# Kernel tuning notes

Hardware: AMD Instinct MI355X
Metric: run time of the kernel (lower is better)

The kernel has to match this reference:

```python
import jax, jax.numpy as jnp
import numpy as np

N = 32768   # total nodes
B = 128     # graphs
L = 256     # nodes per graph (equal-size graphs -> pad_sequence == reshape)
F = 768     # num_features
NH = 256    # nhid
H = 128     # lstm hidden per direction (nhid // 2)
E = 524288  # edges
C = 2       # num_classes


def setup_inputs() -> dict:
    key = jax.random.key(0)
    ks = jax.random.split(key, 16)
    def w(k, shape, fan_in):
        return jax.random.normal(k, shape, jnp.float32) / np.sqrt(fan_in)
    x = jax.random.normal(ks[0], (N, F), jnp.float32)
    edge_index = jax.random.randint(ks[1], (2, E), 0, N)
    batch = jnp.repeat(jnp.arange(B), L)  # sorted graph ids, L nodes per graph
    return {
        "x": x,
        "edge_index": edge_index,
        "batch": batch,
        "W_gcn": w(ks[2], (F, NH), F),
        "b_gcn": jnp.zeros((NH,), jnp.float32),
        # LSTM layer 0: [dir, 4H, Din], gate order i,f,g,o (PyTorch)
        "lstm0_Wih": w(ks[3], (2, 4 * H, F), F),
        "lstm0_Whh": w(ks[4], (2, 4 * H, H), H),
        "lstm0_b": jnp.zeros((2, 4 * H), jnp.float32),
        # LSTM layer 1: input = 2H (bidirectional concat)
        "lstm1_Wih": w(ks[5], (2, 4 * H, 2 * H), 2 * H),
        "lstm1_Whh": w(ks[6], (2, 4 * H, H), H),
        "lstm1_b": jnp.zeros((2, 4 * H), jnp.float32),
        "W_seq": w(ks[7], (NH, NH), NH),
        "b_seq": jnp.zeros((NH,), jnp.float32),
        "W1": w(ks[8], (2 * NH, NH), 2 * NH),
        "b1": jnp.zeros((NH,), jnp.float32),
        "W2": w(ks[9], (NH, C), NH),
        "b2": jnp.zeros((C,), jnp.float32),
    }


def _lstm_dir(xs, Wih, Whh, b, reverse):
    # xs: [Bt, L, Din] -> hidden seq [Bt, L, H]
    Hh = Whh.shape[-1]
    def step(carry, xt):
        h, c = carry
        g = xt @ Wih.T + h @ Whh.T + b
        i, f, gg, o = jnp.split(g, 4, axis=-1)
        c = jax.nn.sigmoid(f) * c + jax.nn.sigmoid(i) * jnp.tanh(gg)
        h = jax.nn.sigmoid(o) * jnp.tanh(c)
        return (h, c), h
    x_t = jnp.swapaxes(xs, 0, 1)  # [L, Bt, Din]
    init = (jnp.zeros((xs.shape[0], Hh), xs.dtype),
            jnp.zeros((xs.shape[0], Hh), xs.dtype))
    _, hs = jax.lax.scan(step, init, x_t, reverse=reverse)
    return jnp.swapaxes(hs, 0, 1)


def _lstm_bidir(xs, Wih, Whh, b):
    fwd = _lstm_dir(xs, Wih[0], Whh[0], b[0], False)
    bwd = _lstm_dir(xs, Wih[1], Whh[1], b[1], True)
    return jnp.concatenate([fwd, bwd], axis=-1)


def reference(x, edge_index, batch, W_gcn, b_gcn,
              lstm0_Wih, lstm0_Whh, lstm0_b,
              lstm1_Wih, lstm1_Whh, lstm1_b,
              W_seq, b_seq, W1, b1, W2, b2):
    n = x.shape[0]
    # --- GCNConv (add self loops, symmetric norm) ---
    loops = jnp.arange(n)
    row = jnp.concatenate([edge_index[0], loops])
    col = jnp.concatenate([edge_index[1], loops])
    deg = jax.ops.segment_sum(jnp.ones_like(col, x.dtype), col, num_segments=n)
    dinv = jnp.where(deg > 0, jax.lax.rsqrt(deg), 0.0)
    norm = dinv[row] * dinv[col]
    h = x @ W_gcn                                   # [N, NH]
    agg = jax.ops.segment_sum(h[row] * norm[:, None], col, num_segments=n)
    x_graph = jax.nn.relu(agg + b_gcn)
    # --- global max pool per graph ---
    x_graph = jax.ops.segment_max(x_graph, batch, num_segments=B)  # [B, NH]
    # --- unbatch + pad_sequence (equal-size graphs -> reshape) ---
    seq_x = x.reshape(B, L, F)
    # --- bidirectional 2-layer LSTM ---
    seq_x = _lstm_bidir(seq_x, lstm0_Wih, lstm0_Whh, lstm0_b)  # [B, L, 2H]
    seq_x = _lstm_bidir(seq_x, lstm1_Wih, lstm1_Whh, lstm1_b)  # [B, L, 2H]
    seq_x = seq_x[:, 0, :]                                      # pre_padding=False -> first step
    # dropout is identity in eval mode
    x_seq = jax.nn.leaky_relu(seq_x @ W_seq + b_seq, negative_slope=0.01)
    out = jnp.concatenate([x_graph, x_seq], axis=1)             # [B, 2*NH]
    out = jax.nn.relu(out @ W1 + b1)
    return jax.nn.log_softmax(out @ W2 + b2, axis=-1)
```

## Files before the change

### kernel.cpp

```cpp
#include <hip/hip_runtime.h>
#include <math.h>


namespace {

constexpr int kN  = 32768;
constexpr int kB  = 128;
constexpr int kL  = 256;
constexpr int kF  = 768;
constexpr int kNH = 256;
constexpr int kH  = 128;
constexpr int kE  = 524288;

typedef __attribute__((ext_vector_type(8))) short bf16x8;
typedef __attribute__((ext_vector_type(4))) float f32x4;
typedef __attribute__((address_space(3))) unsigned int lds_u32;
typedef __attribute__((address_space(1))) unsigned int glb_u32;

__device__ __forceinline__ float sigf(float x)  { return 1.f / (1.f + __expf(-x)); }
__device__ __forceinline__ float tanh_f(float x){ return 1.f - 2.f / (1.f + __expf(2.f * x)); }

__device__ __forceinline__ unsigned short f2bf(float f) {
  unsigned int u = __float_as_uint(f);
  u = u + 0x7fffu + ((u >> 16) & 1u);
  return (unsigned short)(u >> 16);
}
__device__ __forceinline__ float bf2f(unsigned short h) {
  return __uint_as_float((unsigned int)h << 16);
}


__global__ void count_edges(const int* __restrict__ col, int* __restrict__ cnt) {
  int e = blockIdx.x * 256 + threadIdx.x;
  if (e < kE) atomicAdd(&cnt[col[e]], 1);
}

__global__ void scan_dinv(const int* __restrict__ cnt, int* __restrict__ offs,
                          int* __restrict__ cursor, float* __restrict__ dinv) {
  __shared__ int part[1024];
  int t = threadIdx.x;
  int base = t * 32;
  int loc[32];
  int s = 0;
#pragma unroll
  for (int i = 0; i < 32; i++) { loc[i] = cnt[base + i]; s += loc[i]; }
  part[t] = s;
  __syncthreads();
  for (int d = 1; d < 1024; d <<= 1) {
    int v = part[t];
    int add = (t >= d) ? part[t - d] : 0;
    __syncthreads();
    part[t] = v + add;
    __syncthreads();
  }
  int run = (t == 0) ? 0 : part[t - 1];
#pragma unroll
  for (int i = 0; i < 32; i++) {
    offs[base + i] = run;
    cursor[base + i] = run;
    dinv[base + i] = rsqrtf((float)(loc[i] + 1));
    run += loc[i];
  }
  if (t == 1023) offs[kN] = run;
}

__global__ void fill_csr(const int* __restrict__ row, const int* __restrict__ col,
                         int* __restrict__ cursor, int* __restrict__ elist) {
  int e = blockIdx.x * 256 + threadIdx.x;
  if (e < kE) {
    int c = col[e];
    int p = atomicAdd(&cursor[c], 1);
    elist[p] = row[e];
  }
}


__global__ void convert_bt(const float* __restrict__ W, unsigned short* __restrict__ hi,
                           unsigned short* __restrict__ lo, int Nn, int Kk, int trans) {
  int idx = blockIdx.x * 256 + threadIdx.x;
  if (idx >= Nn * Kk) return;
  int n = idx / Kk, k = idx - n * Kk;
  float f = trans ? W[(size_t)k * Nn + n] : W[idx];
  unsigned short h = f2bf(f);
  hi[idx] = h;
  lo[idx] = f2bf(f - bf2f(h));
}

__global__ __launch_bounds__(256, 2) void gemm3(const float* __restrict__ A,
                                                const unsigned short* __restrict__ Bhi,
                                                const unsigned short* __restrict__ Blo,
                                                float* __restrict__ C,
                                                int M, int N, int K) {
  __shared__ __align__(16) char lds[32768];
  const int tid = threadIdx.x;
  const int lane = tid & 63;
  const int w = tid >> 6, wr = w >> 1, wc = w & 1;
  const int m0 = blockIdx.y * 128, n0 = blockIdx.x * 128;

  f32x4 acc[4][4];
#pragma unroll
  for (int i = 0; i < 4; i++)
#pragma unroll
    for (int j = 0; j < 4; j++) acc[i][j] = (f32x4)0.f;

  const float* aptr[4];
  int aoff[4];
#pragma unroll
  for (int i = 0; i < 4; i++) {
    int f = tid + i * 256;
    int row = f >> 3, kq4 = f & 7;
    aptr[i] = A + (size_t)(m0 + row) * K + kq4 * 4;
    int sub = row >> 4, r = row & 15, q = kq4 >> 1, hs = kq4 & 1;
    aoff[i] = sub * 1024 + (q * 16 + r) * 16 + hs * 8;
  }
  const unsigned short* bsrc[4];
  int boff[4];
#pragma unroll
  for (int j = 0; j < 4; j++) {
    int id = w * 4 + j;
    int isLo = id >> 3, sub = id & 7;
    const unsigned short* Bp = isLo ? Blo : Bhi;
    bsrc[j] = Bp + (size_t)(n0 + sub * 16 + (lane & 15)) * K + (lane >> 4) * 8;
    boff[j] = 16384 + isLo * 8192 + sub * 1024;
  }

  for (int k0 = 0; k0 < K; k0 += 32) {
#pragma unroll
    for (int j = 0; j < 4; j++) {
      __builtin_amdgcn_global_load_lds((const glb_u32*)bsrc[j],
                                       (lds_u32*)(lds + boff[j]), 16, 0, 0);
      bsrc[j] += 32;
    }
#pragma unroll
    for (int i = 0; i < 4; i++) {
      f32x4 v = *(const f32x4*)(aptr[i]);
      aptr[i] += 32;
      unsigned short h0 = f2bf(v.x), h1 = f2bf(v.y), h2 = f2bf(v.z), h3 = f2bf(v.w);
      unsigned short g0 = f2bf(v.x - bf2f(h0)), g1 = f2bf(v.y - bf2f(h1));
      unsigned short g2 = f2bf(v.z - bf2f(h2)), g3 = f2bf(v.w - bf2f(h3));
      uint2 hv, lv;
      hv.x = (unsigned int)h0 | ((unsigned int)h1 << 16);
      hv.y = (unsigned int)h2 | ((unsigned int)h3 << 16);
      lv.x = (unsigned int)g0 | ((unsigned int)g1 << 16);
      lv.y = (unsigned int)g2 | ((unsigned int)g3 << 16);
      *(uint2*)(lds + aoff[i]) = hv;
      *(uint2*)(lds + aoff[i] + 8192) = lv;
    }
    __syncthreads();

    const bf16x8* L = (const bf16x8*)lds;
    bf16x8 ah[4], al[4], bh[4], bl[4];
#pragma unroll
    for (int m = 0; m < 4; m++) {
      ah[m] = L[(wr * 4 + m) * 64 + lane];
      al[m] = L[512 + (wr * 4 + m) * 64 + lane];
    }
#pragma unroll
    for (int n = 0; n < 4; n++) {
      bh[n] = L[1024 + (wc * 4 + n) * 64 + lane];
      bl[n] = L[1536 + (wc * 4 + n) * 64 + lane];
    }
#pragma unroll
    for (int m = 0; m < 4; m++)
#pragma unroll
      for (int n = 0; n < 4; n++) {
        acc[m][n] = __builtin_amdgcn_mfma_f32_16x16x32_bf16(ah[m], bh[n], acc[m][n], 0, 0, 0);
        acc[m][n] = __builtin_amdgcn_mfma_f32_16x16x32_bf16(ah[m], bl[n], acc[m][n], 0, 0, 0);
        acc[m][n] = __builtin_amdgcn_mfma_f32_16x16x32_bf16(al[m], bh[n], acc[m][n], 0, 0, 0);
      }
    __syncthreads();
  }

#pragma unroll
  for (int m = 0; m < 4; m++)
#pragma unroll
    for (int n = 0; n < 4; n++) {
      int r0 = m0 + wr * 64 + m * 16 + (lane >> 4) * 4;
      int cc = n0 + wc * 64 + n * 16 + (lane & 15);
#pragma unroll
      for (int j = 0; j < 4; j++)
        C[(size_t)(r0 + j) * N + cc] = acc[m][n][j];
    }
}


__global__ __launch_bounds__(256) void gcn_gather(const float* __restrict__ hg,
                                                  const int* __restrict__ offs,
                                                  const int* __restrict__ elist,
                                                  const float* __restrict__ dinv,
                                                  const float* __restrict__ bgcn,
                                                  float* __restrict__ out) {
  int n = blockIdx.x, j = threadIdx.x;
  float di = dinv[n];
  float acc = hg[(size_t)n * kNH + j] * (di * di);
  int s = offs[n], e = offs[n + 1];
  int p = s;
  for (; p + 4 <= e; p += 4) {
    int r0 = elist[p], r1 = elist[p + 1], r2 = elist[p + 2], r3 = elist[p + 3];
    float w0 = di * dinv[r0], w1 = di * dinv[r1], w2 = di * dinv[r2], w3 = di * dinv[r3];
    float v0 = hg[(size_t)r0 * kNH + j], v1 = hg[(size_t)r1 * kNH + j];
    float v2 = hg[(size_t)r2 * kNH + j], v3 = hg[(size_t)r3 * kNH + j];
    acc = fmaf(v0, w0, acc); acc = fmaf(v1, w1, acc);
    acc = fmaf(v2, w2, acc); acc = fmaf(v3, w3, acc);
  }
  for (; p < e; p++) {
    int r = elist[p];
    acc = fmaf(hg[(size_t)r * kNH + j], di * dinv[r], acc);
  }
  acc += bgcn[j];
  out[(size_t)n * kNH + j] = fmaxf(acc, 0.f);
}

__global__ __launch_bounds__(256) void segmax(const float* __restrict__ xg_full,
                                              float* __restrict__ x_graph) {
  int g = blockIdx.x, j = threadIdx.x;
  const float* base = xg_full + (size_t)g * kL * kNH + j;
  float m0 = -1e30f, m1 = -1e30f, m2 = -1e30f, m3 = -1e30f;
  for (int t = 0; t < kL; t += 4) {
    m0 = fmaxf(m0, base[(size_t)(t + 0) * kNH]);
    m1 = fmaxf(m1, base[(size_t)(t + 1) * kNH]);
    m2 = fmaxf(m2, base[(size_t)(t + 2) * kNH]);
    m3 = fmaxf(m3, base[(size_t)(t + 3) * kNH]);
  }
  x_graph[g * kNH + j] = fmaxf(fmaxf(m0, m1), fmaxf(m2, m3));
}


__global__ __launch_bounds__(512, 2) void lstm_rec(const float* __restrict__ Z, int zstride,
                                                   const float* __restrict__ Whh2,
                                                   const float* __restrict__ bias2,
                                                   float* __restrict__ Y0,
                                                   float* __restrict__ hfin, int mode) {
  __shared__ __align__(16) float hbuf[kH];
  __shared__ float gbuf[512];
  int b, dir;
  if (mode == 0) { dir = blockIdx.x >> 7; b = blockIdx.x & 127; }
  else           { dir = 1;               b = blockIdx.x; }
  const bool rev = (dir == 1);
  int g = threadIdx.x;

  const float* wrow = Whh2 + (size_t)dir * 512 * kH + (size_t)g * kH;
  float w[kH];
#pragma unroll
  for (int k = 0; k < kH / 4; k++) {
    float4 v = *(const float4*)(wrow + 4 * k);
    w[4 * k + 0] = v.x; w[4 * k + 1] = v.y; w[4 * k + 2] = v.z; w[4 * k + 3] = v.w;
  }
  float bg = bias2[dir * 512 + g];
  int zcol = (mode == 0) ? dir * 512 : 0;

  if (g < kH) hbuf[g] = 0.f;
  float c = 0.f;
  __syncthreads();

  const float* zp = Z + (size_t)(b * kL + (rev ? kL - 1 : 0)) * zstride + zcol + g;
  long zinc = rev ? -(long)zstride : (long)zstride;
  float zt = *zp;

  for (int t = 0; t < kL; t++) {
    int tt = rev ? (kL - 1 - t) : t;
    float znext = 0.f;
    if (t < kL - 1) znext = zp[zinc];
    zp += zinc;

    float acc = zt + bg;
#pragma unroll
    for (int kk = 0; kk < kH / 4; kk++) {
      float4 h4 = *(const float4*)&hbuf[kk * 4];
      acc = fmaf(w[4 * kk + 0], h4.x, acc);
      acc = fmaf(w[4 * kk + 1], h4.y, acc);
      acc = fmaf(w[4 * kk + 2], h4.z, acc);
      acc = fmaf(w[4 * kk + 3], h4.w, acc);
    }
    float a = (g < 256 || g >= 384) ? sigf(acc) : tanh_f(acc);
    gbuf[g] = a;
    __syncthreads();
    if (g < kH) {
      float ig = gbuf[g], fg = gbuf[kH + g], gg = gbuf[2 * kH + g], og = gbuf[3 * kH + g];
      c = fg * c + ig * gg;
      float hn = og * tanh_f(c);
      hbuf[g] = hn;
      if (mode == 0) Y0[(size_t)(b * kL + tt) * kNH + dir * kH + g] = hn;
    }
    __syncthreads();
    zt = znext;
  }
  if (mode == 1 && g < kH) hfin[b * kH + g] = hbuf[g];
}


__global__ __launch_bounds__(256) void head(const float* __restrict__ Y0,
                                            const float* __restrict__ h1b,
                                            const float* __restrict__ Wih1f,
                                            const float* __restrict__ b1f,
                                            const float* __restrict__ xgraph,
                                            const float* __restrict__ Wseq,
                                            const float* __restrict__ bseq,
                                            const float* __restrict__ W1,
                                            const float* __restrict__ b1,
                                            const float* __restrict__ W2,
                                            const float* __restrict__ b2,
                                            float* __restrict__ out) {
  int b = blockIdx.x, t = threadIdx.x;
  __shared__ __align__(16) float x0[kNH];
  __shared__ float gl[512];
  __shared__ __align__(16) float seq[kNH];
  __shared__ __align__(16) float v[512];
  __shared__ __align__(16) float o1[kNH];
  __shared__ float red[512];

  x0[t] = Y0[(size_t)(b * kL) * kNH + t];
  if (t >= kH) seq[t] = h1b[b * kH + (t - kH)];
  __syncthreads();

#pragma unroll
  for (int half = 0; half < 2; half++) {
    int g = t + half * 256;
    const float* wr = Wih1f + (size_t)g * kNH;
    float acc = b1f[g];
#pragma unroll 8
    for (int k = 0; k < kNH; k += 4) {
      float4 xv = *(const float4*)&x0[k];
      float4 wv = *(const float4*)(wr + k);
      acc = fmaf(xv.x, wv.x, acc); acc = fmaf(xv.y, wv.y, acc);
      acc = fmaf(xv.z, wv.z, acc); acc = fmaf(xv.w, wv.w, acc);
    }
    gl[g] = acc;
  }
  __syncthreads();
  if (t < kH) {
    float ig = sigf(gl[t]);
    float gg = tanh_f(gl[2 * kH + t]);
    float og = sigf(gl[3 * kH + t]);
    float c = ig * gg;
    seq[t] = og * tanh_f(c);
  }
  v[t] = xgraph[b * kNH + t];
  __syncthreads();

  {
    float acc = bseq[t];
#pragma unroll 4
    for (int k = 0; k < kNH; k++) acc = fmaf(seq[k], Wseq[(size_t)k * kNH + t], acc);
    v[kNH + t] = (acc > 0.f) ? acc : 0.01f * acc;
  }
  __syncthreads();

  {
    float acc = b1[t];
#pragma unroll 4
    for (int k = 0; k < 512; k++) acc = fmaf(v[k], W1[(size_t)k * kNH + t], acc);
    o1[t] = fmaxf(acc, 0.f);
  }
  __syncthreads();

  red[t]       = o1[t] * W2[t * 2 + 0];
  red[kNH + t] = o1[t] * W2[t * 2 + 1];
  __syncthreads();
  for (int s = 128; s > 0; s >>= 1) {
    if (t < s) { red[t] += red[t + s]; red[kNH + t] += red[kNH + t + s]; }
    __syncthreads();
  }
  if (t == 0) {
    float z0 = red[0] + b2[0], z1 = red[kNH] + b2[1];
    float m = fmaxf(z0, z1);
    float lse = m + logf(__expf(z0 - m) + __expf(z1 - m));
    out[b * 2 + 0] = z0 - lse;
    out[b * 2 + 1] = z1 - lse;
  }
}

}

extern "C" void kernel_launch(void* const* d_in, const int* in_sizes, int n_in,
                              void* d_out, int out_size, void* d_ws, size_t ws_size,
                              hipStream_t stream) {
  const float* x     = (const float*)d_in[0];
  const int*   ei    = (const int*)d_in[1];
  const float* Wgcn  = (const float*)d_in[3];
  const float* bgcn  = (const float*)d_in[4];
  const float* l0Wih = (const float*)d_in[5];
  const float* l0Whh = (const float*)d_in[6];
  const float* l0b   = (const float*)d_in[7];
  const float* l1Wih = (const float*)d_in[8];
  const float* l1Whh = (const float*)d_in[9];
  const float* l1b   = (const float*)d_in[10];
  const float* Wseq  = (const float*)d_in[11];
  const float* bseq  = (const float*)d_in[12];
  const float* W1    = (const float*)d_in[13];
  const float* b1    = (const float*)d_in[14];
  const float* W2    = (const float*)d_in[15];
  const float* b2    = (const float*)d_in[16];
  float* out = (float*)d_out;
  char* ws = (char*)d_ws;

  float* Z0     = (float*)(ws);
  float* Y0     = (float*)(ws + 134217728UL);
  float* xgraph = (float*)(ws + 134217728UL + 33554432UL);
  float* h1b    = (float*)(ws + 134217728UL + 33554432UL + 131072UL);
  float* hgcn   = Z0;
  float* xgfull = (float*)(ws + 33554432UL);
  int*   cnt    = (int*)(ws + 67108864UL);
  int*   offs   = (int*)(ws + 67108864UL + 1048576UL);
  int*   cursor = (int*)(ws + 67108864UL + 2097152UL);
  int*   elist  = (int*)(ws + 67108864UL + 3145728UL);
  float* dinv   = (float*)(ws + 67108864UL + 6291456UL);
  float* Z1b    = Z0;

  unsigned short* gWhi = (unsigned short*)(ws + 78643200UL);
  unsigned short* gWlo = (unsigned short*)(ws + 78643200UL + 393216UL);
  unsigned short* l0hi = (unsigned short*)(ws + 134217728UL);
  unsigned short* l0lo = (unsigned short*)(ws + 134217728UL + 1572864UL);
  unsigned short* l1hi = (unsigned short*)(ws + 104857600UL);
  unsigned short* l1lo = (unsigned short*)(ws + 104857600UL + 262144UL);

  const int* erow = ei;
  const int* ecol = ei + kE;

  hipMemsetAsync(cnt, 0, kN * sizeof(int), stream);
  count_edges<<<kE / 256, 256, 0, stream>>>(ecol, cnt);
  scan_dinv<<<1, 1024, 0, stream>>>(cnt, offs, cursor, dinv);
  fill_csr<<<kE / 256, 256, 0, stream>>>(erow, ecol, cursor, elist);
  convert_bt<<<(kNH * kF + 255) / 256, 256, 0, stream>>>(Wgcn, gWhi, gWlo, kNH, kF, 1);
  gemm3<<<dim3(kNH / 128, kN / 128), 256, 0, stream>>>(x, gWhi, gWlo, hgcn, kN, kNH, kF);
  gcn_gather<<<kN, 256, 0, stream>>>(hgcn, offs, elist, dinv, bgcn, xgfull);
  segmax<<<kB, 256, 0, stream>>>(xgfull, xgraph);

  convert_bt<<<(1024 * kF + 255) / 256, 256, 0, stream>>>(l0Wih, l0hi, l0lo, 1024, kF, 0);
  gemm3<<<dim3(1024 / 128, kN / 128), 256, 0, stream>>>(x, l0hi, l0lo, Z0, kN, 1024, kF);
  lstm_rec<<<256, 512, 0, stream>>>(Z0, 1024, l0Whh, l0b, Y0, nullptr, 0);
  convert_bt<<<(512 * kNH + 255) / 256, 256, 0, stream>>>(l1Wih + 512 * 256, l1hi, l1lo,
                                                          512, kNH, 0);
  gemm3<<<dim3(512 / 128, kN / 128), 256, 0, stream>>>(Y0, l1hi, l1lo, Z1b, kN, 512, kNH);
  lstm_rec<<<128, 512, 0, stream>>>(Z1b, 512, l1Whh, l1b, nullptr, h1b, 1);

  head<<<kB, 256, 0, stream>>>(Y0, h1b, l1Wih, l1b, xgraph, Wseq, bseq, W1, b1, W2, b2, out);
}
```

Before: 1.125 ms.

## Restructure LSTM recurrence: 4-lane k-split per hidden unit with shuffle reduction, double-buffered h

Measured after the change: 1.094 ms. 2.8% less time.

```diff
diff --git a/kernel.cpp b/kernel.cpp
--- a/kernel.cpp
+++ b/kernel.cpp
@@ -85,6 +85,7 @@
   hi[idx] = h;
   lo[idx] = f2bf(f - bf2f(h));
 }
+
 
 __global__ __launch_bounds__(256, 2) void gemm3(const float* __restrict__ A,
                                                 const unsigned short* __restrict__ Bhi,
@@ -225,67 +226,94 @@
   x_graph[g * kNH + j] = fmaxf(fmaxf(m0, m1), fmaxf(m2, m3));
 }
 
-
 __global__ __launch_bounds__(512, 2) void lstm_rec(const float* __restrict__ Z, int zstride,
                                                    const float* __restrict__ Whh2,
                                                    const float* __restrict__ bias2,
                                                    float* __restrict__ Y0,
                                                    float* __restrict__ hfin, int mode) {
-  __shared__ __align__(16) float hbuf[kH];
-  __shared__ float gbuf[512];
+  __shared__ __align__(16) float hbuf[2][kH];
   int b, dir;
   if (mode == 0) { dir = blockIdx.x >> 7; b = blockIdx.x & 127; }
   else           { dir = 1;               b = blockIdx.x; }
   const bool rev = (dir == 1);
-  int g = threadIdx.x;
-
-  const float* wrow = Whh2 + (size_t)dir * 512 * kH + (size_t)g * kH;
-  float w[kH];
-#pragma unroll
-  for (int k = 0; k < kH / 4; k++) {
-    float4 v = *(const float4*)(wrow + 4 * k);
-    w[4 * k + 0] = v.x; w[4 * k + 1] = v.y; w[4 * k + 2] = v.z; w[4 * k + 3] = v.w;
-  }
-  float bg = bias2[dir * 512 + g];
-  int zcol = (mode == 0) ? dir * 512 : 0;
-
-  if (g < kH) hbuf[g] = 0.f;
-  float c = 0.f;
-  __syncthreads();
-
-  const float* zp = Z + (size_t)(b * kL + (rev ? kL - 1 : 0)) * zstride + zcol + g;
-  long zinc = rev ? -(long)zstride : (long)zstride;
+  const int t0 = threadIdx.x;
+  const int j = t0 >> 2;
+  const int ks = t0 & 3;
+
+  float w[4][32];
+  {
+    const float* wb = Whh2 + (size_t)dir * 512 * kH + (size_t)j * kH + ks * 32;
+#pragma unroll
+    for (int q = 0; q < 4; q++) {
+      const float* wr = wb + (size_t)q * kH * kH;
+#pragma unroll
+      for (int kk = 0; kk < 8; kk++) {
+        float4 v = *(const float4*)(wr + kk * 4);
+        w[q][kk * 4 + 0] = v.x; w[q][kk * 4 + 1] = v.y;
+        w[q][kk * 4 + 2] = v.z; w[q][kk * 4 + 3] = v.w;
+      }
+    }
+  }
+#pragma unroll
+  for (int q = 0; q < 4; q++)
+#pragma unroll
+    for (int kk = 0; kk < 32; kk++) asm volatile("" : "+v"(w[q][kk]));
+
+  const float bg = bias2[dir * 512 + ks * kH + j];
+  const int zcol = (mode == 0) ? dir * 512 : 0;
+  float c = 0.f, hn = 0.f;
+
+  if (ks == 0) hbuf[0][j] = 0.f;
+
+  const float* zp = Z + (size_t)(b * kL + (rev ? kL - 1 : 0)) * zstride + zcol + ks * kH + j;
+  const long zinc = rev ? -(long)zstride : (long)zstride;
   float zt = *zp;
+  __syncthreads();
 
   for (int t = 0; t < kL; t++) {
-    int tt = rev ? (kL - 1 - t) : t;
+    const int tt = rev ? (kL - 1 - t) : t;
     float znext = 0.f;
     if (t < kL - 1) znext = zp[zinc];
     zp += zinc;
-
-    float acc = zt + bg;
-#pragma unroll
-    for (int kk = 0; kk < kH / 4; kk++) {
-      float4 h4 = *(const float4*)&hbuf[kk * 4];
-      acc = fmaf(w[4 * kk + 0], h4.x, acc);
-      acc = fmaf(w[4 * kk + 1], h4.y, acc);
-      acc = fmaf(w[4 * kk + 2], h4.z, acc);
-      acc = fmaf(w[4 * kk + 3], h4.w, acc);
-    }
-    float a = (g < 256 || g >= 384) ? sigf(acc) : tanh_f(acc);
-    gbuf[g] = a;
-    __syncthreads();
-    if (g < kH) {
-      float ig = gbuf[g], fg = gbuf[kH + g], gg = gbuf[2 * kH + g], og = gbuf[3 * kH + g];
-      c = fg * c + ig * gg;
-      float hn = og * tanh_f(c);
-      hbuf[g] = hn;
-      if (mode == 0) Y0[(size_t)(b * kL + tt) * kNH + dir * kH + g] = hn;
+    const int cur = t & 1;
+
+    float h[32];
+    const float4* hp = (const float4*)&hbuf[cur][ks * 32];
+#pragma unroll
+    for (int kk = 0; kk < 8; kk++) {
+      float4 v = hp[kk];
+      h[kk * 4 + 0] = v.x; h[kk * 4 + 1] = v.y; h[kk * 4 + 2] = v.z; h[kk * 4 + 3] = v.w;
+    }
+
+    float a0 = 0.f, a1 = 0.f, a2 = 0.f, a3 = 0.f;
+#pragma unroll
+    for (int kk = 0; kk < 32; kk++) {
+      a0 = fmaf(w[0][kk], h[kk], a0);
+      a1 = fmaf(w[1][kk], h[kk], a1);
+      a2 = fmaf(w[2][kk], h[kk], a2);
+      a3 = fmaf(w[3][kk], h[kk], a3);
+    }
+    const float zb = zt + bg;
+    a0 += (ks == 0) ? zb : 0.f;
+    a1 += (ks == 1) ? zb : 0.f;
+    a2 += (ks == 2) ? zb : 0.f;
+    a3 += (ks == 3) ? zb : 0.f;
+    a0 += __shfl_xor(a0, 1); a1 += __shfl_xor(a1, 1);
+    a2 += __shfl_xor(a2, 1); a3 += __shfl_xor(a3, 1);
+    a0 += __shfl_xor(a0, 2); a1 += __shfl_xor(a1, 2);
+    a2 += __shfl_xor(a2, 2); a3 += __shfl_xor(a3, 2);
+
+    const float ig = sigf(a0), fg = sigf(a1), gg = tanh_f(a2), og = sigf(a3);
+    c = fg * c + ig * gg;
+    hn = og * tanh_f(c);
+    if (ks == 0) {
+      hbuf[cur ^ 1][j] = hn;
+      if (mode == 0) Y0[(size_t)(b * kL + tt) * kNH + dir * kH + j] = hn;
     }
     __syncthreads();
     zt = znext;
   }
-  if (mode == 1 && g < kH) hfin[b * kH + g] = hbuf[g];
+  if (mode == 1 && ks == 0) hfin[b * kH + j] = hn;
 }
 
 
```
